# Kernel optimization log

Measured on AMD Instinct MI355X. Metric: run time of the kernel, lower is better.

## Reference

```python
import jax, jax.numpy as jnp
import numpy as np

N, E, D = 100000, 1000000, 128  # nodes, edges, feature/embedding dim


def setup_inputs() -> dict:
    key = jax.random.key(0)
    ks = jax.random.split(key, 8)
    s = 1.0 / np.sqrt(D)
    return {
        "x": jax.random.normal(ks[0], (N, D), jnp.float32),
        "edge_index": jax.random.randint(ks[1], (2, E), 0, N, jnp.int32),
        # layer 1: lin_l (with bias) on aggregated neighbors, lin_r (no bias) on root
        "W1_l": jax.random.normal(ks[2], (D, D), jnp.float32) * s,
        "b1_l": jnp.zeros((D,), jnp.float32),
        "W1_r": jax.random.normal(ks[3], (D, D), jnp.float32) * s,
        # layer 2
        "W2_l": jax.random.normal(ks[4], (D, D), jnp.float32) * s,
        "b2_l": jnp.zeros((D,), jnp.float32),
        "W2_r": jax.random.normal(ks[5], (D, D), jnp.float32) * s,
    }


def _sage_conv(x, src, dst, Wl, bl, Wr):
    # PyG SAGEConv (aggr='mean'): out = lin_l(mean_{j->i} x_j) + lin_r(x_i)
    msgs = x[src]                                            # [E, D] gather
    agg = jax.ops.segment_sum(msgs, dst, num_segments=N)     # [N, D] scatter-add
    cnt = jax.ops.segment_sum(jnp.ones((src.shape[0],), x.dtype), dst,
                              num_segments=N)                # [N]
    mean = agg / jnp.maximum(cnt, 1.0)[:, None]
    return mean @ Wl + bl + x @ Wr


def reference(x, edge_index, W1_l, b1_l, W1_r, W2_l, b2_l, W2_r):
    src, dst = edge_index[0], edge_index[1]
    h = jax.nn.relu(_sage_conv(x, src, dst, W1_l, b1_l, W1_r))  # dropout inactive (eval)
    return _sage_conv(h, src, dst, W2_l, b2_l, W2_r)            # [N, D] embeddings
```

## Files before the change

kernel.cpp:

```cpp
#include <hip/hip_runtime.h>

#define D 128
constexpr int NPB   = 128;
constexpr int BCAP  = 2048;
constexpr int SEGB  = 2048;
constexpr int KMAX  = 1024;

typedef __bf16 bf16x8 __attribute__((ext_vector_type(8)));
typedef float f32x4 __attribute__((ext_vector_type(4)));
typedef int intv4 __attribute__((ext_vector_type(4)));

__device__ __forceinline__ unsigned short f2bf(float f) {
    unsigned int u = __float_as_uint(f);
    unsigned int r = (u + 0x7fffu + ((u >> 16) & 1u)) >> 16;
    return (unsigned short)r;
}
__device__ __forceinline__ unsigned pack2(float a, float b) {
    return (unsigned)f2bf(a) | ((unsigned)f2bf(b) << 16);
}

__global__ __launch_bounds__(256) void front_kernel(
    const int* __restrict__ src, const int* __restrict__ dst,
    unsigned long long* __restrict__ bucket, int* __restrict__ bCur,
    int E, int K, int NB,
    const float* __restrict__ W1l, const float* __restrict__ W1r,
    const float* __restrict__ W2l, const float* __restrict__ W2r,
    unsigned short* __restrict__ Wpack,
    const float* __restrict__ xin, unsigned short* __restrict__ xb, int n4)
{
    const int t = threadIdx.x;
    if (blockIdx.x < (unsigned)NB) {
        __shared__ int lcnt[KMAX], lbase[KMAX];
        for (int i = t; i < K; i += 256) lcnt[i] = 0;
        __syncthreads();

        const int e0 = blockIdx.x * SEGB + t * 8;
        intv4 d0, d1, s0, s1;
        if (e0 + 8 <= E) {
            d0 = __builtin_nontemporal_load(reinterpret_cast<const intv4*>(dst + e0));
            d1 = __builtin_nontemporal_load(reinterpret_cast<const intv4*>(dst + e0 + 4));
            s0 = __builtin_nontemporal_load(reinterpret_cast<const intv4*>(src + e0));
            s1 = __builtin_nontemporal_load(reinterpret_cast<const intv4*>(src + e0 + 4));
        } else {
#pragma unroll
            for (int k = 0; k < 4; ++k) {
                d0[k] = (e0 + k < E) ? dst[e0 + k] : -1;
                d1[k] = (e0 + 4 + k < E) ? dst[e0 + 4 + k] : -1;
                s0[k] = (e0 + k < E) ? src[e0 + k] : 0;
                s1[k] = (e0 + 4 + k < E) ? src[e0 + 4 + k] : 0;
            }
        }
#pragma unroll
        for (int k = 0; k < 8; ++k) {
            int d = (k < 4) ? d0[k] : d1[k - 4];
            if (d >= 0) atomicAdd(&lcnt[d >> 7], 1);
        }
        __syncthreads();
        for (int i = t; i < K; i += 256) {
            int c = lcnt[i];
            lbase[i] = c ? atomicAdd(&bCur[i], c) : 0;
            lcnt[i] = 0;
        }
        __syncthreads();
#pragma unroll
        for (int k = 0; k < 8; ++k) {
            int d = (k < 4) ? d0[k] : d1[k - 4];
            int s = (k < 4) ? s0[k] : s1[k - 4];
            if (d >= 0) {
                int b = d >> 7;
                int p = lbase[b] + atomicAdd(&lcnt[b], 1);
                if (p < BCAP)
                    bucket[(size_t)b * BCAP + p] =
                        ((unsigned long long)(unsigned)s << 32) | (unsigned)d;
            }
        }
    } else if (blockIdx.x < (unsigned)(NB + 32)) {
        int b = (blockIdx.x - NB) * 4 + (t >> 6);
        int l = t & 63;
        int layer = b >> 6, wsel = (b >> 5) & 1, kt = (b >> 3) & 3, ct = b & 7;
        const float* W = layer ? (wsel ? W2r : W2l) : (wsel ? W1r : W1l);
        int k0  = kt * 32 + (l >> 4) * 8;
        int col = ct * 16 + (l & 15);
        unsigned short tmp[8];
#pragma unroll
        for (int j = 0; j < 8; ++j) tmp[j] = f2bf(W[(k0 + j) * D + col]);
        size_t fbase = (((size_t)layer * 64 + wsel * 32 + kt * 8 + ct) * 64 + l) * 8;
        uint4 o;
        o.x = (unsigned)tmp[0] | ((unsigned)tmp[1] << 16);
        o.y = (unsigned)tmp[2] | ((unsigned)tmp[3] << 16);
        o.z = (unsigned)tmp[4] | ((unsigned)tmp[5] << 16);
        o.w = (unsigned)tmp[6] | ((unsigned)tmp[7] << 16);
        *reinterpret_cast<uint4*>(Wpack + fbase) = o;
    } else {
        int i = (blockIdx.x - NB - 32) * 256 + t;
        if (i < n4) {
            float4 v = reinterpret_cast<const float4*>(xin)[i];
            ushort4 o;
            o.x = f2bf(v.x); o.y = f2bf(v.y); o.z = f2bf(v.z); o.w = f2bf(v.w);
            reinterpret_cast<ushort4*>(xb)[i] = o;
        }
    }
}

__global__ __launch_bounds__(256) void csrbuild_kernel(
    const unsigned long long* __restrict__ bucket, const int* __restrict__ bCur,
    int2* __restrict__ offe, int* __restrict__ csr, int K, int N)
{
    __shared__ unsigned long long ebuf[BCAP];
    __shared__ int lhist[NPB], sc[NPB], lcur[NPB];
    __shared__ int red[256];
    const int t = threadIdx.x;
    const int b = blockIdx.x;

    int s = 0;
    for (int i = t; i < b; i += 256) s += bCur[i];
    red[t] = s;
    __syncthreads();
    for (int o = 128; o; o >>= 1) {
        if (t < o) red[t] += red[t + o];
        __syncthreads();
    }
    const int gbase = red[0];
    const int cnt = min(bCur[b], BCAP);

    if (t < NPB) lhist[t] = 0;
    __syncthreads();

    const unsigned long long* bp = bucket + (size_t)b * BCAP;
    for (int i = t; i < cnt; i += 256) {
        unsigned long long e = bp[i];
        ebuf[i] = e;
        atomicAdd(&lhist[(int)(e & 127ULL)], 1);
    }
    __syncthreads();

    if (t < NPB) sc[t] = lhist[t];
    __syncthreads();
    for (int o = 1; o < NPB; o <<= 1) {
        int y = 0;
        if (t < NPB && t >= o) y = sc[t - o];
        __syncthreads();
        if (t < NPB) sc[t] += y;
        __syncthreads();
    }
    if (t < NPB) {
        int node = b * NPB + t;
        int excl = sc[t] - lhist[t];
        lcur[t] = excl;
        if (node < N) offe[node] = make_int2(gbase + excl, gbase + sc[t]);
    }
    __syncthreads();

    for (int i = t; i < cnt; i += 256) {
        unsigned long long e = ebuf[i];
        int dl = (int)(e & 127ULL);
        int p = gbase + atomicAdd(&lcur[dl], 1);
        csr[p] = (int)(e >> 32);
    }
}

__global__ __launch_bounds__(256) void gather4_bf16(
    const unsigned short* __restrict__ feat, const int2* __restrict__ offe,
    const int* __restrict__ csr,
    unsigned short* __restrict__ mean, int N)
{
    int tid = blockIdx.x * 256 + threadIdx.x;
    int n   = tid >> 4;
    int q   = tid & 15;
    if (n >= N) return;
    int2 be = offe[n];
    int b = be.x, e = be.y;
    const uint4* fp = reinterpret_cast<const uint4*>(feat) + q;

    float acc[8];
#pragma unroll
    for (int i = 0; i < 8; ++i) acc[i] = 0.f;

    int j = b;
    for (; j + 3 < e; j += 4) {
        int s0 = __builtin_nontemporal_load(csr + j);
        int s1 = __builtin_nontemporal_load(csr + j + 1);
        int s2 = __builtin_nontemporal_load(csr + j + 2);
        int s3 = __builtin_nontemporal_load(csr + j + 3);
        uint4 v0 = fp[(size_t)s0 * 16];
        uint4 v1 = fp[(size_t)s1 * 16];
        uint4 v2 = fp[(size_t)s2 * 16];
        uint4 v3 = fp[(size_t)s3 * 16];
        const unsigned* u0 = &v0.x;
        const unsigned* u1 = &v1.x;
        const unsigned* u2 = &v2.x;
        const unsigned* u3 = &v3.x;
#pragma unroll
        for (int i = 0; i < 4; ++i) {
            acc[2 * i]     += __uint_as_float(u0[i] << 16) + __uint_as_float(u1[i] << 16)
                            + __uint_as_float(u2[i] << 16) + __uint_as_float(u3[i] << 16);
            acc[2 * i + 1] += __uint_as_float(u0[i] & 0xffff0000u) + __uint_as_float(u1[i] & 0xffff0000u)
                            + __uint_as_float(u2[i] & 0xffff0000u) + __uint_as_float(u3[i] & 0xffff0000u);
        }
    }
    for (; j < e; ++j) {
        uint4 v0 = fp[(size_t)csr[j] * 16];
        const unsigned* u0 = &v0.x;
#pragma unroll
        for (int i = 0; i < 4; ++i) {
            acc[2 * i]     += __uint_as_float(u0[i] << 16);
            acc[2 * i + 1] += __uint_as_float(u0[i] & 0xffff0000u);
        }
    }
    float invd = 1.0f / (float)max(e - b, 1);
#pragma unroll
    for (int i = 0; i < 8; ++i) acc[i] *= invd;
    uint4 o;
    o.x = pack2(acc[0], acc[1]);
    o.y = pack2(acc[2], acc[3]);
    o.z = pack2(acc[4], acc[5]);
    o.w = pack2(acc[6], acc[7]);
    *reinterpret_cast<uint4*>(mean + (size_t)n * D + q * 8) = o;
}

template <int RELU, int OUT_BF16>
__global__ __launch_bounds__(256, 2) void sage_mfma(
    const unsigned short* __restrict__ meanb,
    const unsigned short* __restrict__ xb,
    const unsigned short* __restrict__ Wpack,
    const float* __restrict__ bl,
    void* __restrict__ outv, int Mtiles, int TPB)
{
    __shared__ __align__(16) char sbuf[2][8192];
    const int t    = threadIdx.x;
    const int lane = t & 63;
    const int wc   = t >> 6;
    const int l15  = lane & 15;
    const int lhi  = lane >> 4;

    bf16x8 bfrag[2][8];
#pragma unroll
    for (int ktt = 0; ktt < 8; ++ktt) {
        int wsel = ktt >> 2, kt = ktt & 3;
#pragma unroll
        for (int c = 0; c < 2; ++c) {
            int ct = wc * 2 + c;
            size_t fbase = ((size_t)(wsel * 32 + kt * 8 + ct) * 64 + lane) * 8;
            bfrag[c][ktt] = *reinterpret_cast<const bf16x8*>(Wpack + fbase);
        }
    }
    float bias[2];
    bias[0] = bl[wc * 32 + l15];
    bias[1] = bl[wc * 32 + 16 + l15];

    int tile0 = blockIdx.x * TPB;
    if (tile0 >= Mtiles) return;
    int tend = min(tile0 + TPB, Mtiles);

    const int sr = t >> 4;
    const int sq = t & 15;
    const int ss = sq ^ (sr & 7);
    char* dstM = &sbuf[0][sr * 256 + ss * 16];
    char* dstX = &sbuf[0][4096 + sr * 256 + ss * 16];

    {
        size_t gofs = (size_t)(tile0 * 16 + sr) * D + sq * 8;
        *reinterpret_cast<uint4*>(dstM) = *reinterpret_cast<const uint4*>(meanb + gofs);
        *reinterpret_cast<uint4*>(dstX) = *reinterpret_cast<const uint4*>(xb + gofs);
    }
    int cur = 0;

    for (int it = tile0; it < tend; ++it) {
        __syncthreads();
        const bool pf = (it + 1 < tend);
        uint4 mv, xv;
        if (pf) {
            size_t gofs = (size_t)((it + 1) * 16 + sr) * D + sq * 8;
            mv = *reinterpret_cast<const uint4*>(meanb + gofs);
            xv = *reinterpret_cast<const uint4*>(xb + gofs);
        }

        f32x4 acc0 = {0.f, 0.f, 0.f, 0.f};
        f32x4 acc1 = {0.f, 0.f, 0.f, 0.f};
        const char* base = sbuf[cur];
#pragma unroll
        for (int ktt = 0; ktt < 8; ++ktt) {
            int p = ktt >> 2, kt = ktt & 3;
            int q = kt * 4 + lhi;
            int byteoff = p * 4096 + l15 * 256 + ((q ^ (l15 & 7)) * 16);
            bf16x8 a = *reinterpret_cast<const bf16x8*>(base + byteoff);
            acc0 = __builtin_amdgcn_mfma_f32_16x16x32_bf16(a, bfrag[0][ktt], acc0, 0, 0, 0);
            acc1 = __builtin_amdgcn_mfma_f32_16x16x32_bf16(a, bfrag[1][ktt], acc1, 0, 0, 0);
        }

        int rbase = it * 16 + lhi * 4;
#pragma unroll
        for (int c = 0; c < 2; ++c) {
            int col = wc * 32 + c * 16 + l15;
            const f32x4& a = c ? acc1 : acc0;
#pragma unroll
            for (int r = 0; r < 4; ++r) {
                float v = a[r] + bias[c];
                if (RELU) v = fmaxf(v, 0.f);
                if (OUT_BF16) {
                    ((unsigned short*)outv)[(size_t)(rbase + r) * D + col] = f2bf(v);
                } else {
                    ((float*)outv)[(size_t)(rbase + r) * D + col] = v;
                }
            }
        }

        if (pf) {
            char* dM = dstM + (cur ^ 1) * 8192;
            char* dX = dstX + (cur ^ 1) * 8192;
            *reinterpret_cast<uint4*>(dM) = mv;
            *reinterpret_cast<uint4*>(dX) = xv;
            cur ^= 1;
        }
    }
}

extern "C" void kernel_launch(void* const* d_in, const int* in_sizes, int n_in,
                              void* d_out, int out_size, void* d_ws, size_t ws_size,
                              hipStream_t stream) {
    const float* x   = (const float*)d_in[0];
    const int*   ei  = (const int*)d_in[1];
    const float* W1l = (const float*)d_in[2];
    const float* b1l = (const float*)d_in[3];
    const float* W1r = (const float*)d_in[4];
    const float* W2l = (const float*)d_in[5];
    const float* b2l = (const float*)d_in[6];
    const float* W2r = (const float*)d_in[7];
    float* out = (float*)d_out;

    const int N = in_sizes[0] / D;
    const int E = in_sizes[1] / 2;
    const int* src = ei;
    const int* dst = ei + E;

    unsigned short* xb    = (unsigned short*)d_ws;
    unsigned short* meanb = xb + (size_t)N * D;
    unsigned short* hb    = meanb + (size_t)N * D;
    unsigned short* Wpack = hb + (size_t)N * D;
    int* bCur     = (int*)(Wpack + 65536);
    int2* offe    = (int2*)(bCur + KMAX);
    int* csr_src  = (int*)(offe + N);

    unsigned long long* bucket = (unsigned long long*)hb;

    const int K = (N + NPB - 1) / NPB;
    const int Mtiles  = (N + 15) / 16;
    const int TPB     = 8;
    const int gemmGrid = (Mtiles + TPB - 1) / TPB;
    const int gatherBlocks = (int)(((long long)N * 16 + 255) / 256);
    const int NB = (E + SEGB - 1) / SEGB;
    const int n4 = N * D / 4;
    const int convBlocks = (n4 + 255) / 256;

    hipMemsetAsync(bCur, 0, (size_t)K * sizeof(int), stream);
    front_kernel<<<NB + 32 + convBlocks, 256, 0, stream>>>(
        src, dst, bucket, bCur, E, K, NB,
        W1l, W1r, W2l, W2r, Wpack, x, xb, n4);
    csrbuild_kernel<<<K, 256, 0, stream>>>(bucket, bCur, offe, csr_src, K, N);

    gather4_bf16<<<gatherBlocks, 256, 0, stream>>>(xb, offe, csr_src, meanb, N);
    sage_mfma<1, 1><<<gemmGrid, 256, 0, stream>>>(meanb, xb, Wpack, b1l, hb, Mtiles, TPB);

    gather4_bf16<<<gatherBlocks, 256, 0, stream>>>(hb, offe, csr_src, meanb, N);
    sage_mfma<0, 0><<<gemmGrid, 256, 0, stream>>>(meanb, hb, Wpack + 32768, b2l, out, Mtiles, TPB);
}
```

Measured before the change: 166.5 us.

## Quantize node features to int8 with per-row scales for neighbor gather

Node features are stored as int8 with one float scale per row (128 values), built in the front kernel for x and in a new quantH kernel for h. The gather kernels then read 8 bytes per lane instead of 16 and dequantize with the row scale while accumulating. The aim is to halve the bytes moved by the bandwidth-bound random gathers. The cost is an extra quantization pass, a scale load per edge, and lower accuracy. BCAP is shrunk so the int8 x buffer fits after the bucket region in the hb workspace.

```diff
diff --git a/kernel.cpp b/kernel.cpp
--- a/kernel.cpp
+++ b/kernel.cpp
@@ -2,7 +2,7 @@
 
 #define D 128
 constexpr int NPB   = 128;
-constexpr int BCAP  = 2048;
+constexpr int BCAP  = 1536;
 constexpr int SEGB  = 2048;
 constexpr int KMAX  = 1024;
 
@@ -17,6 +17,10 @@
 }
 __device__ __forceinline__ unsigned pack2(float a, float b) {
     return (unsigned)f2bf(a) | ((unsigned)f2bf(b) << 16);
+}
+__device__ __forceinline__ int q8clamp(float v) {
+    int q = __float2int_rn(v);
+    return min(max(q, -127), 127);
 }
 
 __global__ __launch_bounds__(256) void front_kernel(
@@ -26,7 +30,8 @@
     const float* __restrict__ W1l, const float* __restrict__ W1r,
     const float* __restrict__ W2l, const float* __restrict__ W2r,
     unsigned short* __restrict__ Wpack,
-    const float* __restrict__ xin, unsigned short* __restrict__ xb, int n4)
+    const float* __restrict__ xin, unsigned short* __restrict__ xb,
+    unsigned* __restrict__ xq, float* __restrict__ sx, int n4)
 {
     const int t = threadIdx.x;
     if (blockIdx.x < (unsigned)NB) {
@@ -98,6 +103,19 @@
             ushort4 o;
             o.x = f2bf(v.x); o.y = f2bf(v.y); o.z = f2bf(v.z); o.w = f2bf(v.w);
             reinterpret_cast<ushort4*>(xb)[i] = o;
+            float am = fmaxf(fmaxf(fabsf(v.x), fabsf(v.y)),
+                             fmaxf(fabsf(v.z), fabsf(v.w)));
+#pragma unroll
+            for (int off = 1; off < 32; off <<= 1)
+                am = fmaxf(am, __shfl_xor(am, off, 32));
+            am = fmaxf(am, 1e-20f);
+            float inv = 127.0f / am;
+            unsigned q = ((unsigned)(q8clamp(v.x * inv) & 0xff))
+                       | ((unsigned)(q8clamp(v.y * inv) & 0xff) << 8)
+                       | ((unsigned)(q8clamp(v.z * inv) & 0xff) << 16)
+                       | ((unsigned)(q8clamp(v.w * inv) & 0xff) << 24);
+            xq[i] = q;
+            if ((t & 31) == 0) sx[i >> 5] = am / 127.0f;
         }
     }
 }
@@ -159,9 +177,58 @@
     }
 }
 
-__global__ __launch_bounds__(256) void gather4_bf16(
-    const unsigned short* __restrict__ feat, const int2* __restrict__ offe,
-    const int* __restrict__ csr,
+__global__ __launch_bounds__(256) void quantH_kernel(
+    const unsigned short* __restrict__ hb, uint2* __restrict__ hq,
+    float* __restrict__ sh, int N)
+{
+    int idx = blockIdx.x * 256 + threadIdx.x;
+    int n = idx >> 4;
+    int q = idx & 15;
+    if (n >= N) return;
+    uint4 v = *reinterpret_cast<const uint4*>(hb + (size_t)n * D + q * 8);
+    const unsigned* u = &v.x;
+    float f[8];
+#pragma unroll
+    for (int i = 0; i < 4; ++i) {
+        f[2 * i]     = __uint_as_float(u[i] << 16);
+        f[2 * i + 1] = __uint_as_float(u[i] & 0xffff0000u);
+    }
+    float am = 0.f;
+#pragma unroll
+    for (int i = 0; i < 8; ++i) am = fmaxf(am, fabsf(f[i]));
+#pragma unroll
+    for (int off = 1; off < 16; off <<= 1)
+        am = fmaxf(am, __shfl_xor(am, off, 16));
+    am = fmaxf(am, 1e-20f);
+    float inv = 127.0f / am;
+    uint2 o;
+    o.x = ((unsigned)(q8clamp(f[0] * inv) & 0xff))
+        | ((unsigned)(q8clamp(f[1] * inv) & 0xff) << 8)
+        | ((unsigned)(q8clamp(f[2] * inv) & 0xff) << 16)
+        | ((unsigned)(q8clamp(f[3] * inv) & 0xff) << 24);
+    o.y = ((unsigned)(q8clamp(f[4] * inv) & 0xff))
+        | ((unsigned)(q8clamp(f[5] * inv) & 0xff) << 8)
+        | ((unsigned)(q8clamp(f[6] * inv) & 0xff) << 16)
+        | ((unsigned)(q8clamp(f[7] * inv) & 0xff) << 24);
+    hq[(size_t)n * 16 + q] = o;
+    if (q == 0) sh[n] = am / 127.0f;
+}
+
+__device__ __forceinline__ void acc8(uint2 v, float sc, float* acc) {
+#pragma unroll
+    for (int w = 0; w < 2; ++w) {
+        unsigned x = w ? v.y : v.x;
+#pragma unroll
+        for (int b = 0; b < 4; ++b) {
+            int e = (int)((signed char)((x >> (8 * b)) & 0xffu));
+            acc[4 * w + b] = fmaf((float)e, sc, acc[4 * w + b]);
+        }
+    }
+}
+
+__global__ __launch_bounds__(256) void gather8_i8(
+    const uint2* __restrict__ q8, const float* __restrict__ scales,
+    const int2* __restrict__ offe, const int* __restrict__ csr,
     unsigned short* __restrict__ mean, int N)
 {
     int tid = blockIdx.x * 256 + threadIdx.x;
@@ -170,7 +237,7 @@
     if (n >= N) return;
     int2 be = offe[n];
     int b = be.x, e = be.y;
-    const uint4* fp = reinterpret_cast<const uint4*>(feat) + q;
+    const uint2* fp = q8 + q;
 
     float acc[8];
 #pragma unroll
@@ -182,30 +249,23 @@
         int s1 = __builtin_nontemporal_load(csr + j + 1);
         int s2 = __builtin_nontemporal_load(csr + j + 2);
         int s3 = __builtin_nontemporal_load(csr + j + 3);
-        uint4 v0 = fp[(size_t)s0 * 16];
-        uint4 v1 = fp[(size_t)s1 * 16];
-        uint4 v2 = fp[(size_t)s2 * 16];
-        uint4 v3 = fp[(size_t)s3 * 16];
-        const unsigned* u0 = &v0.x;
-        const unsigned* u1 = &v1.x;
-        const unsigned* u2 = &v2.x;
-        const unsigned* u3 = &v3.x;
-#pragma unroll
-        for (int i = 0; i < 4; ++i) {
-            acc[2 * i]     += __uint_as_float(u0[i] << 16) + __uint_as_float(u1[i] << 16)
-                            + __uint_as_float(u2[i] << 16) + __uint_as_float(u3[i] << 16);
-            acc[2 * i + 1] += __uint_as_float(u0[i] & 0xffff0000u) + __uint_as_float(u1[i] & 0xffff0000u)
-                            + __uint_as_float(u2[i] & 0xffff0000u) + __uint_as_float(u3[i] & 0xffff0000u);
-        }
+        uint2 v0 = fp[(size_t)s0 * 16];
+        uint2 v1 = fp[(size_t)s1 * 16];
+        uint2 v2 = fp[(size_t)s2 * 16];
+        uint2 v3 = fp[(size_t)s3 * 16];
+        float c0 = scales[s0];
+        float c1 = scales[s1];
+        float c2 = scales[s2];
+        float c3 = scales[s3];
+        acc8(v0, c0, acc);
+        acc8(v1, c1, acc);
+        acc8(v2, c2, acc);
+        acc8(v3, c3, acc);
     }
     for (; j < e; ++j) {
-        uint4 v0 = fp[(size_t)csr[j] * 16];
-        const unsigned* u0 = &v0.x;
-#pragma unroll
-        for (int i = 0; i < 4; ++i) {
-            acc[2 * i]     += __uint_as_float(u0[i] << 16);
-            acc[2 * i + 1] += __uint_as_float(u0[i] & 0xffff0000u);
-        }
+        int s0 = csr[j];
+        uint2 v0 = fp[(size_t)s0 * 16];
+        acc8(v0, scales[s0], acc);
     }
     float invd = 1.0f / (float)max(e - b, 1);
 #pragma unroll
@@ -333,6 +393,8 @@
     const int* src = ei;
     const int* dst = ei + E;
 
+    const int K = (N + NPB - 1) / NPB;
+
     unsigned short* xb    = (unsigned short*)d_ws;
     unsigned short* meanb = xb + (size_t)N * D;
     unsigned short* hb    = meanb + (size_t)N * D;
@@ -340,10 +402,13 @@
     int* bCur     = (int*)(Wpack + 65536);
     int2* offe    = (int2*)(bCur + KMAX);
     int* csr_src  = (int*)(offe + N);
+    float* sx     = (float*)(csr_src + E);
+    float* sh     = sx + N;
 
     unsigned long long* bucket = (unsigned long long*)hb;
-
-    const int K = (N + NPB - 1) / NPB;
+    unsigned* xq = (unsigned*)((char*)hb + (size_t)K * BCAP * 8);
+    uint2* hq = (uint2*)xb;
+
     const int Mtiles  = (N + 15) / 16;
     const int TPB     = 8;
     const int gemmGrid = (Mtiles + TPB - 1) / TPB;
@@ -351,16 +416,21 @@
     const int NB = (E + SEGB - 1) / SEGB;
     const int n4 = N * D / 4;
     const int convBlocks = (n4 + 255) / 256;
+    const int quantBlocks = (int)(((long long)N * 16 + 255) / 256);
 
     hipMemsetAsync(bCur, 0, (size_t)K * sizeof(int), stream);
     front_kernel<<<NB + 32 + convBlocks, 256, 0, stream>>>(
         src, dst, bucket, bCur, E, K, NB,
-        W1l, W1r, W2l, W2r, Wpack, x, xb, n4);
+        W1l, W1r, W2l, W2r, Wpack, x, xb, xq, sx, n4);
     csrbuild_kernel<<<K, 256, 0, stream>>>(bucket, bCur, offe, csr_src, K, N);
 
-    gather4_bf16<<<gatherBlocks, 256, 0, stream>>>(xb, offe, csr_src, meanb, N);
+    gather8_i8<<<gatherBlocks, 256, 0, stream>>>(
+        (const uint2*)xq, sx, offe, csr_src, meanb, N);
     sage_mfma<1, 1><<<gemmGrid, 256, 0, stream>>>(meanb, xb, Wpack, b1l, hb, Mtiles, TPB);
 
-    gather4_bf16<<<gatherBlocks, 256, 0, stream>>>(hb, offe, csr_src, meanb, N);
+    quantH_kernel<<<quantBlocks, 256, 0, stream>>>(hb, hq, sh, N);
+
+    gather8_i8<<<gatherBlocks, 256, 0, stream>>>(
+        hq, sh, offe, csr_src, meanb, N);
     sage_mfma<0, 0><<<gemmGrid, 256, 0, stream>>>(meanb, hb, Wpack + 32768, b2l, out, Mtiles, TPB);
 }
```

New measurement: 161.5 us. 1.03x faster.
